# Optimization experiments

Measured on AMD Instinct MI355X. Metric: run time of the kernel, lower is better.

Reference implementation:

```python
import jax, jax.numpy as jnp
import numpy as np

K = 7     # kernel_size
H_HEADS = 16  # h


def setup_inputs() -> dict:
    key = jax.random.key(0)
    k1, k2 = jax.random.split(key)
    B, S, D = 8, 2048, 1024
    x = jax.random.normal(k1, (B, S, D), dtype=jnp.float32)
    W = jax.random.normal(k2, (D, K * H_HEADS), dtype=jnp.float32) * (1.0 / np.sqrt(D))
    b = jnp.zeros((K * H_HEADS,), dtype=jnp.float32)
    return {"x": x, "W": W, "b": b}


def reference(x, W, b):
    B, S, D = x.shape
    L = S - K + 1  # number of output positions
    rep = D // H_HEADS
    # dynamic kernels from positions K-1..S-1: [B, L, K, h]
    kern = (x[:, K - 1:] @ W + b).reshape(B, L, K, H_HEADS)
    kern = jax.nn.softmax(kern, axis=-2)
    # tf.tile([1,1,1,rep]): repeat the whole h-block rep times -> [B, L, K, D]
    kern = jnp.tile(kern, (1, 1, 1, rep))
    # sliding windows: windows[b, i, k] = x[b, i + k]  -> [B, L, K, D]
    idx = jnp.arange(L)[:, None] + jnp.arange(K)[None, :]
    windows = x[:, idx]
    # weighted mean over the kernel axis (tf.reduce_mean)
    out = jnp.mean(kern * windows, axis=2)  # [B, L, D]
    return out
```

## Files before the change

### kernel.cpp

```cpp
#include <hip/hip_runtime.h>


#define KK 7
#define HH 16
#define DD 1024
#define SS 2048
#define LL 2042
#define NO 112
#define TL 16
#define WTF_BYTES (7 * 32 * 64 * 8 * 2)

typedef __attribute__((ext_vector_type(8))) short bf16x8;
typedef __attribute__((ext_vector_type(4))) float f32x4;

__device__ __forceinline__ unsigned short f2bf(float f) {
    unsigned u = __builtin_bit_cast(unsigned, f);
    u += 0x7fffu + ((u >> 16) & 1u);
    return (unsigned short)(u >> 16);
}
__device__ __forceinline__ unsigned bfpack(float lo, float hi) {
    return (unsigned)f2bf(lo) | ((unsigned)f2bf(hi) << 16);
}
__device__ __forceinline__ float bflo(unsigned u) {
    return __builtin_bit_cast(float, u << 16);
}
__device__ __forceinline__ float bfhi(unsigned u) {
    return __builtin_bit_cast(float, u & 0xffff0000u);
}

__global__ void wprep(const float* __restrict__ W, unsigned short* __restrict__ wtf) {
    const int bx = blockIdx.x;
    const int lane = threadIdx.x;
    const int i = bx >> 5, ks = bx & 31;
    const int frow = lane & 15, fq = lane >> 4;
    const int col = i * 16 + frow;
    const int k0 = ks * 32 + fq * 8;
    unsigned p[4];
#pragma unroll
    for (int j = 0; j < 4; ++j) {
        float a = W[(size_t)(k0 + 2 * j) * NO + col];
        float b = W[(size_t)(k0 + 2 * j + 1) * NO + col];
        p[j] = bfpack(a, b);
    }
    *(uint4*)(wtf + (size_t)(bx * 64 + lane) * 8) = make_uint4(p[0], p[1], p[2], p[3]);
}

template <bool WSOK>
__global__ __launch_bounds__(512, 2)
void dlconv(const float* __restrict__ x, const float* __restrict__ W,
            const float* __restrict__ bias, const unsigned short* __restrict__ wtf,
            float* __restrict__ out)
{
    __shared__ __align__(16) unsigned char smem[52480];
    float* Lg = (float*)(smem + 45056);
    float* P  = (float*)(smem + 45056);
    const int t  = threadIdx.x;
    const int lb = blockIdx.x, b = blockIdx.y;
    const int l0 = lb * TL;
    const float* xb = x + (size_t)b * SS * DD;

#pragma unroll
    for (int s = 0; s < 11; ++s) {
        int idx = t + 512 * s;
        int rr = idx >> 8, c4 = idx & 255;
        int gr = l0 + rr; gr = gr < SS ? gr : SS - 1;
        float4 v = *(const float4*)(xb + (size_t)gr * DD + c4 * 4);
        int addr = rr * 2048 + ((c4 * 8) ^ ((rr & 7) << 4));
        *(uint2*)(smem + addr) = make_uint2(bfpack(v.x, v.y), bfpack(v.z, v.w));
    }
    __syncthreads();

    const int lane = t & 63, wid = t >> 6;
    const int frow = lane & 15, fq = lane >> 4;
    f32x4 acc = (f32x4)0.f;
    if (wid < 7) {
        const int arr = 6 + frow;
        const int abase = arr * 2048;
        const int aswz = (arr & 7) << 4;
#pragma unroll 8
        for (int ks = 0; ks < 32; ++ks) {
            bf16x8 af = *(const bf16x8*)(smem + abase + ((ks * 64 + fq * 16) ^ aswz));
            bf16x8 bf;
            if constexpr (WSOK) {
                bf = *(const bf16x8*)(wtf + (size_t)((wid * 32 + ks) * 64 + lane) * 8);
            } else {
                const float* wp = W + (size_t)(ks * 32 + fq * 8) * NO + wid * 16 + frow;
                short e0 = (short)f2bf(wp[0 * NO]), e1 = (short)f2bf(wp[1 * NO]);
                short e2 = (short)f2bf(wp[2 * NO]), e3 = (short)f2bf(wp[3 * NO]);
                short e4 = (short)f2bf(wp[4 * NO]), e5 = (short)f2bf(wp[5 * NO]);
                short e6 = (short)f2bf(wp[6 * NO]), e7 = (short)f2bf(wp[7 * NO]);
                bf = bf16x8{e0, e1, e2, e3, e4, e5, e6, e7};
            }
            acc = __builtin_amdgcn_mfma_f32_16x16x32_bf16(af, bf, acc, 0, 0, 0);
        }
        float bi = bias[wid * 16 + frow];
#pragma unroll
        for (int reg = 0; reg < 4; ++reg)
            Lg[(fq * 4 + reg) * 116 + wid * 16 + frow] = acc[reg] + bi;
    }
    __syncthreads();

    float v[KK];
    if (t < 256) {
        const int r = t >> 4, h = t & 15;
        float m = -1e30f;
#pragma unroll
        for (int i = 0; i < KK; ++i) {
            v[i] = Lg[r * 116 + i * 16 + h];
            m = fmaxf(m, v[i]);
        }
        float ssum = 0.f;
#pragma unroll
        for (int i = 0; i < KK; ++i) { v[i] = __expf(v[i] - m); ssum += v[i]; }
        float inv = 1.f / (7.f * ssum);
#pragma unroll
        for (int i = 0; i < KK; ++i) v[i] *= inv;
    }
    __syncthreads();
    if (t < 256) {
        const int r = t >> 4, h = t & 15;
#pragma unroll
        for (int i = 0; i < KK; ++i) P[(r * KK + i) * 16 + h] = v[i];
    }
    __syncthreads();

    const int rg = t >> 8;
    const int cc = t & 255;
    const int hs = (cc & 3) << 2;
    const int coff = cc * 8;
#pragma unroll
    for (int q = 0; q < 8; ++q) {
        int row = rg * 8 + q;
        if (l0 + row < LL) {
            f32x4 o = (f32x4)0.f;
#pragma unroll
            for (int k = 0; k < KK; ++k) {
                int rr = row + k;
                uint2 u = *(const uint2*)(smem + rr * 2048 + (coff ^ ((rr & 7) << 4)));
                f32x4 pv = *(const f32x4*)(P + (row * KK + k) * 16 + hs);
                o.x += pv.x * bflo(u.x);
                o.y += pv.y * bfhi(u.x);
                o.z += pv.z * bflo(u.y);
                o.w += pv.w * bfhi(u.y);
            }
            *(f32x4*)(out + ((size_t)b * LL + l0 + row) * DD + cc * 4) = o;
        }
    }
}

extern "C" void kernel_launch(void* const* d_in, const int* in_sizes, int n_in,
                              void* d_out, int out_size, void* d_ws, size_t ws_size,
                              hipStream_t stream) {
    const float* x    = (const float*)d_in[0];
    const float* W    = (const float*)d_in[1];
    const float* bias = (const float*)d_in[2];
    float* out        = (float*)d_out;
    dim3 grid((LL + TL - 1) / TL, 8);
    const bool wsok = (ws_size >= (size_t)WTF_BYTES) && d_ws != nullptr;
    if (wsok) {
        unsigned short* wtf = (unsigned short*)d_ws;
        wprep<<<224, 64, 0, stream>>>(W, wtf);
        dlconv<true><<<grid, 512, 0, stream>>>(x, W, bias, wtf, out);
    } else {
        dlconv<false><<<grid, 512, 0, stream>>>(x, W, bias, nullptr, out);
    }
}
```

Measured before the change: 40.53 us.

## Shrink LDS tile to 16 rows, read halo rows directly from global

The shared-memory tile now holds only the 16 rows needed for the projection GEMM (rows l0+6..l0+21) instead of 22 rows. The six halo rows used by the first output rows are loaded straight from global memory in fp32 by the first thread group. The softmax weights are written back in place over the logits, which removes a buffer and one barrier. LDS use drops from about 52KB to 40KB and launch bounds are raised to allow more blocks per CU. The cost is extra global loads and uneven work between the two thread groups.

```diff
diff --git a/kernel.cpp b/kernel.cpp
--- a/kernel.cpp
+++ b/kernel.cpp
@@ -46,37 +46,35 @@
 }
 
 template <bool WSOK>
-__global__ __launch_bounds__(512, 2)
+__global__ __launch_bounds__(512, 8)
 void dlconv(const float* __restrict__ x, const float* __restrict__ W,
             const float* __restrict__ bias, const unsigned short* __restrict__ wtf,
             float* __restrict__ out)
 {
-    __shared__ __align__(16) unsigned char smem[52480];
-    float* Lg = (float*)(smem + 45056);
-    float* P  = (float*)(smem + 45056);
+    __shared__ __align__(16) unsigned char smem[40192];
+    float* Lg = (float*)(smem + 32768);
     const int t  = threadIdx.x;
     const int lb = blockIdx.x, b = blockIdx.y;
     const int l0 = lb * TL;
     const float* xb = x + (size_t)b * SS * DD;
 
 #pragma unroll
-    for (int s = 0; s < 11; ++s) {
+    for (int s = 0; s < 8; ++s) {
         int idx = t + 512 * s;
-        int rr = idx >> 8, c4 = idx & 255;
-        int gr = l0 + rr; gr = gr < SS ? gr : SS - 1;
+        int row = idx >> 8, c4 = idx & 255;
+        int gr = l0 + 6 + row; gr = gr < SS ? gr : SS - 1;
         float4 v = *(const float4*)(xb + (size_t)gr * DD + c4 * 4);
-        int addr = rr * 2048 + ((c4 * 8) ^ ((rr & 7) << 4));
+        int addr = row * 2048 + ((c4 * 8) ^ ((row & 7) << 4));
         *(uint2*)(smem + addr) = make_uint2(bfpack(v.x, v.y), bfpack(v.z, v.w));
     }
     __syncthreads();
 
     const int lane = t & 63, wid = t >> 6;
     const int frow = lane & 15, fq = lane >> 4;
-    f32x4 acc = (f32x4)0.f;
     if (wid < 7) {
-        const int arr = 6 + frow;
-        const int abase = arr * 2048;
-        const int aswz = (arr & 7) << 4;
+        const int abase = frow * 2048;
+        const int aswz = (frow & 7) << 4;
+        f32x4 acc = (f32x4)0.f;
 #pragma unroll 8
         for (int ks = 0; ks < 32; ++ks) {
             bf16x8 af = *(const bf16x8*)(smem + abase + ((ks * 64 + fq * 16) ^ aswz));
@@ -100,9 +98,9 @@
     }
     __syncthreads();
 
-    float v[KK];
     if (t < 256) {
         const int r = t >> 4, h = t & 15;
+        float v[KK];
         float m = -1e30f;
 #pragma unroll
         for (int i = 0; i < KK; ++i) {
@@ -114,13 +112,7 @@
         for (int i = 0; i < KK; ++i) { v[i] = __expf(v[i] - m); ssum += v[i]; }
         float inv = 1.f / (7.f * ssum);
 #pragma unroll
-        for (int i = 0; i < KK; ++i) v[i] *= inv;
-    }
-    __syncthreads();
-    if (t < 256) {
-        const int r = t >> 4, h = t & 15;
-#pragma unroll
-        for (int i = 0; i < KK; ++i) P[(r * KK + i) * 16 + h] = v[i];
+        for (int i = 0; i < KK; ++i) Lg[r * 116 + i * 16 + h] = v[i] * inv;
     }
     __syncthreads();
 
@@ -128,22 +120,46 @@
     const int cc = t & 255;
     const int hs = (cc & 3) << 2;
     const int coff = cc * 8;
+    float* orow0 = out + ((size_t)b * LL + l0) * DD + cc * 4;
+
+    if (rg == 0) {
+        f32x4 gx[6];
 #pragma unroll
-    for (int q = 0; q < 8; ++q) {
-        int row = rg * 8 + q;
-        if (l0 + row < LL) {
+        for (int j = 0; j < 6; ++j)
+            gx[j] = *(const f32x4*)(xb + (size_t)(l0 + j) * DD + cc * 4);
+#pragma unroll
+        for (int q = 0; q < 8; ++q) {
             f32x4 o = (f32x4)0.f;
 #pragma unroll
             for (int k = 0; k < KK; ++k) {
-                int rr = row + k;
-                uint2 u = *(const uint2*)(smem + rr * 2048 + (coff ^ ((rr & 7) << 4)));
-                f32x4 pv = *(const f32x4*)(P + (row * KK + k) * 16 + hs);
-                o.x += pv.x * bflo(u.x);
-                o.y += pv.y * bfhi(u.x);
-                o.z += pv.z * bflo(u.y);
-                o.w += pv.w * bfhi(u.y);
+                f32x4 pv = *(const f32x4*)(Lg + q * 116 + k * 16 + hs);
+                if (q + k < 6) {
+                    o += pv * gx[q + k];
+                } else {
+                    int rr = q + k - 6;
+                    uint2 u = *(const uint2*)(smem + rr * 2048 + (coff ^ ((rr & 7) << 4)));
+                    f32x4 xv = { bflo(u.x), bfhi(u.x), bflo(u.y), bfhi(u.y) };
+                    o += pv * xv;
+                }
             }
-            *(f32x4*)(out + ((size_t)b * LL + l0 + row) * DD + cc * 4) = o;
+            *(f32x4*)(orow0 + (size_t)q * DD) = o;
+        }
+    } else {
+#pragma unroll
+        for (int q = 0; q < 8; ++q) {
+            int row = 8 + q;
+            if (l0 + row < LL) {
+                f32x4 o = (f32x4)0.f;
+#pragma unroll
+                for (int k = 0; k < KK; ++k) {
+                    int rr = row + k - 6;
+                    f32x4 pv = *(const f32x4*)(Lg + row * 116 + k * 16 + hs);
+                    uint2 u = *(const uint2*)(smem + rr * 2048 + (coff ^ ((rr & 7) << 4)));
+                    f32x4 xv = { bflo(u.x), bfhi(u.x), bflo(u.y), bfhi(u.y) };
+                    o += pv * xv;
+                }
+                *(f32x4*)(orow0 + (size_t)row * DD) = o;
+            }
         }
     }
 }
```

New measurement: 36.35 us. 10.3% less time.
